# Performance work log

Hardware: AMD Instinct MI355X
Metric: run time of the kernel (lower is better)

## Reference

```python
import jax, jax.numpy as jnp
import numpy as np
import math

B, LQ, LK, D = 16, 2048, 2048, 64

def setup_inputs() -> dict:
    key = jax.random.key(0)
    kq, kk, kv, kn = jax.random.split(key, 4)
    q = jax.random.normal(kq, (B, LQ, D), dtype=jnp.float32)
    k = jax.random.normal(kk, (B, LK, D), dtype=jnp.float32)
    v = jax.random.normal(kv, (B, LK, D), dtype=jnp.float32)
    # valid lengths in [1, LK] so no row is fully masked
    valid_num = jax.random.randint(kn, (B,), 1, LK + 1, dtype=jnp.int32)
    return {"q": q, "k": k, "v": v, "valid_num": valid_num}

def reference(q, k, v, valid_num):
    d = q.shape[-1]
    # [B, LQ, LK] scores
    scores = jnp.einsum('bqd,bkd->bqk', q, k) / math.sqrt(d)
    # 1D valid_num -> same key mask for every query row (matches repeat_interleave)
    key_pos = jnp.arange(k.shape[1], dtype=valid_num.dtype)  # [LK]
    mask = key_pos[None, None, :] < valid_num[:, None, None]  # [B,1,LK] -> broadcast
    scores = jnp.where(mask, scores, -jnp.inf)
    attn = jax.nn.softmax(scores, axis=-1)
    # dropout p=0.0 -> identity (eval/deterministic reference)
    return jnp.einsum('bqk,bkd->bqd', attn, v)
```

## Files before the change

kernel.cpp:

```cpp
#include <hip/hip_runtime.h>


namespace {

constexpr int NB  = 16;
constexpr int SLQ = 2048;
constexpr int SLK = 2048;
constexpr int DH  = 64;
constexpr int KB  = 64;
constexpr int QB  = 64;

typedef _Float16 half8  __attribute__((ext_vector_type(8)));
typedef _Float16 half4  __attribute__((ext_vector_type(4)));
typedef _Float16 half2t __attribute__((ext_vector_type(2)));
typedef float    f32x4  __attribute__((ext_vector_type(4)));

__device__ inline half2t pkrtz(float a, float b) {
    return __builtin_bit_cast(half2t, __builtin_amdgcn_cvt_pkrtz(a, b));
}

__global__ __launch_bounds__(256)
void prepass(const float* __restrict__ kg, const float* __restrict__ vg,
             _Float16* __restrict__ k16, _Float16* __restrict__ v16t)
{
    __shared__ _Float16 VT[DH][72];
    const int t  = threadIdx.x;
    const int b  = blockIdx.x >> 5;
    const int kt = blockIdx.x & 31;

    {
        const size_t base = ((size_t)b * SLK + (size_t)kt * KB) * DH;
        const float* kp = kg + base + t * 16;
        f32x4 a0 = ((const f32x4*)kp)[0], a1 = ((const f32x4*)kp)[1];
        f32x4 a2 = ((const f32x4*)kp)[2], a3 = ((const f32x4*)kp)[3];
        union { half2t h2[8]; uint4 u[2]; } o;
        o.h2[0] = pkrtz(a0[0], a0[1]); o.h2[1] = pkrtz(a0[2], a0[3]);
        o.h2[2] = pkrtz(a1[0], a1[1]); o.h2[3] = pkrtz(a1[2], a1[3]);
        o.h2[4] = pkrtz(a2[0], a2[1]); o.h2[5] = pkrtz(a2[2], a2[3]);
        o.h2[6] = pkrtz(a3[0], a3[1]); o.h2[7] = pkrtz(a3[2], a3[3]);
        uint4* dst = (uint4*)(k16 + base + t * 16);
        dst[0] = o.u[0]; dst[1] = o.u[1];
    }
    {
        const int kr = t >> 2, d0 = (t & 3) * 16;
        const float* vp = vg + ((size_t)b * SLK + (size_t)kt * KB + kr) * DH + d0;
        f32x4 a0 = ((const f32x4*)vp)[0], a1 = ((const f32x4*)vp)[1];
        f32x4 a2 = ((const f32x4*)vp)[2], a3 = ((const f32x4*)vp)[3];
#pragma unroll
        for (int i = 0; i < 4; ++i) {
            VT[d0 + i][kr]      = (_Float16)a0[i];
            VT[d0 + 4 + i][kr]  = (_Float16)a1[i];
            VT[d0 + 8 + i][kr]  = (_Float16)a2[i];
            VT[d0 + 12 + i][kr] = (_Float16)a3[i];
        }
    }
    __syncthreads();
#pragma unroll
    for (int j = 0; j < 2; ++j) {
        const int chunk = t * 2 + j;
        const int d = chunk >> 3, c16 = chunk & 7;
        half8 hv = *(const half8*)&VT[d][c16 * 8];
        *(half8*)(v16t + ((size_t)b * DH + d) * SLK + (size_t)kt * KB + c16 * 8) = hv;
    }
}

__global__ __launch_bounds__(256)
void attn_fwd(const float* __restrict__ qg, const _Float16* __restrict__ k16,
              const _Float16* __restrict__ v16t, const int* __restrict__ vn,
              _Float16* __restrict__ ws_acc, float* __restrict__ ws_ml,
              int nsplit, int tps)
{
    __shared__ _Float16 Kl[KB * DH];
    __shared__ _Float16 Vt[DH * KB];

    const int t   = threadIdx.x;
    const int l   = t & 63;
    const int w   = t >> 6;
    const int q15 = l & 15;
    const int g   = l >> 4;
    const int swz = (q15 & 7) << 3;

    const int bid = blockIdx.x;
    int b, qt, s;
    if (nsplit == 4) {
        const int k3  = bid >> 8;
        const int mm  = (bid >> 4) & 15;
        const int qlo = bid & 15;
        s  = k3 & 3;
        b  = (mm + k3) & 15;
        qt = qlo | ((k3 >> 2) << 4);
    } else {
        b  = ((bid & 15) + 8 * (bid >> 8)) & 15;
        qt = (bid >> 4) & 31;
        s  = 0;
    }

    const int valid = vn[b];
    const int nkt   = (valid + KB - 1) / KB;
    const int kt0   = s * tps;
    if (kt0 >= nkt) return;
    const int kt1   = min(nkt, kt0 + tps);

    const int qrow = qt * QB + w * 16 + q15;

    const float QS = 0.18033688011112042f;

    half8 qf[2];
    {
        const float* qp = qg + ((size_t)b * SLQ + qrow) * DH;
#pragma unroll
        for (int ss = 0; ss < 2; ++ss) {
            const int d0 = 8 * g + 32 * ss;
            f32x4 x = *(const f32x4*)(qp + d0);
            f32x4 y = *(const f32x4*)(qp + d0 + 4);
            half8 h;
#pragma unroll
            for (int i = 0; i < 4; ++i) {
                h[i]     = (_Float16)(x[i] * QS);
                h[i + 4] = (_Float16)(y[i] * QS);
            }
            qf[ss] = h;
        }
    }

    f32x4 acc[4];
#pragma unroll
    for (int i = 0; i < 4; ++i) acc[i] = f32x4{0.f, 0.f, 0.f, 0.f};
    float m = -1e30f, lsum = 0.f;

    const _Float16* k16b = k16 + (size_t)b * SLK * DH;
    const _Float16* v16b = v16t + (size_t)b * DH * SLK;

    for (int kt = kt0; kt < kt1; ++kt) {
        __syncthreads();

#pragma unroll
        for (int j = 0; j < 2; ++j) {
            const int chunk = 2 * t + j;
            const int r = chunk >> 3, c16 = chunk & 7;
            const int sc = (c16 * 8) ^ ((r & 7) << 3);
            uint4 kd = *(const uint4*)(k16b + (size_t)kt * KB * DH + chunk * 8);
            *(uint4*)&Kl[r * 64 + sc] = kd;
            uint4 vd = *(const uint4*)(v16b + (size_t)r * SLK + kt * KB + c16 * 8);
            *(uint4*)&Vt[r * 64 + sc] = vd;
        }
        __syncthreads();

        f32x4 st[4];
#pragma unroll
        for (int mt = 0; mt < 4; ++mt) {
            f32x4 c = f32x4{0.f, 0.f, 0.f, 0.f};
#pragma unroll
            for (int ss = 0; ss < 2; ++ss) {
                half8 a = *(const half8*)&Kl[(16 * mt + q15) * 64 + ((8 * g + 32 * ss) ^ swz)];
                c = __builtin_amdgcn_mfma_f32_16x16x32_f16(a, qf[ss], c, 0, 0, 0);
            }
            st[mt] = c;
        }

        const int krem = valid - kt * KB;
        if (krem < KB) {
#pragma unroll
            for (int mt = 0; mt < 4; ++mt)
#pragma unroll
                for (int r = 0; r < 4; ++r)
                    if (16 * mt + 4 * g + r >= krem) st[mt][r] = -1e30f;
        }

        float tmax = -1e30f;
#pragma unroll
        for (int mt = 0; mt < 4; ++mt)
#pragma unroll
            for (int r = 0; r < 4; ++r) tmax = fmaxf(tmax, st[mt][r]);
        tmax = fmaxf(tmax, __shfl_xor(tmax, 16));
        tmax = fmaxf(tmax, __shfl_xor(tmax, 32));

        const float mn = fmaxf(m, tmax);
        const float sc = __builtin_amdgcn_exp2f(m - mn);

        float p[4][4];
        float ps = 0.f;
#pragma unroll
        for (int mt = 0; mt < 4; ++mt)
#pragma unroll
            for (int r = 0; r < 4; ++r) {
                const float e = __builtin_amdgcn_exp2f(st[mt][r] - mn);
                p[mt][r] = e;
                ps += e;
            }
        ps += __shfl_xor(ps, 16);
        ps += __shfl_xor(ps, 32);
        lsum = lsum * sc + ps;
        m = mn;
#pragma unroll
        for (int mt = 0; mt < 4; ++mt) acc[mt] *= sc;

        half2t pk[4][2];
#pragma unroll
        for (int mt = 0; mt < 4; ++mt)
#pragma unroll
            for (int rr = 0; rr < 2; ++rr)
                pk[mt][rr] = pkrtz(p[mt][2 * rr], p[mt][2 * rr + 1]);

#pragma unroll
        for (int ss = 0; ss < 2; ++ss) {
            union { half2t h2[4]; half8 v; } bf;
            bf.h2[0] = pk[2 * ss][0];
            bf.h2[1] = pk[2 * ss][1];
            bf.h2[2] = pk[2 * ss + 1][0];
            bf.h2[3] = pk[2 * ss + 1][1];
#pragma unroll
            for (int mt = 0; mt < 4; ++mt) {
                union { half4 h4[2]; half8 v; } af;
                af.h4[0] = *(const half4*)&Vt[(16 * mt + q15) * 64 + ((32 * ss + 4 * g) ^ swz)];
                af.h4[1] = *(const half4*)&Vt[(16 * mt + q15) * 64 + ((32 * ss + 16 + 4 * g) ^ swz)];
                acc[mt] = __builtin_amdgcn_mfma_f32_16x16x32_f16(af.v, bf.v, acc[mt], 0, 0, 0);
            }
        }
    }

    const float inv = 1.0f / lsum;
    const size_t row = (size_t)b * SLQ + qrow;
    _Float16* wp = ws_acc + ((size_t)s * NB * SLQ + row) * DH;
#pragma unroll
    for (int mt = 0; mt < 4; ++mt) {
        union { half2t h2[2]; uint2 u; } o;
        o.h2[0] = pkrtz(acc[mt][0] * inv, acc[mt][1] * inv);
        o.h2[1] = pkrtz(acc[mt][2] * inv, acc[mt][3] * inv);
        *(uint2*)(wp + 16 * mt + 4 * g) = o.u;
    }
    if (g == 0)
        *(float2*)(ws_ml + ((size_t)s * NB * SLQ + row) * 2) = make_float2(m, lsum);
}

__global__ __launch_bounds__(256)
void attn_combine(const _Float16* __restrict__ ws_acc, const float* __restrict__ ws_ml,
                  const int* __restrict__ vn, float* __restrict__ og,
                  int nsplit, int tps)
{
    const int tid = blockIdx.x * 256 + threadIdx.x;
    const int row = tid >> 2;
    const int dq  = (tid & 3) << 4;
    const int b   = row >> 11;

    const int valid = vn[b];
    const int nkt   = (valid + KB - 1) / KB;
    const int nact  = min(nsplit, (nkt + tps - 1) / tps);

    float M = -1e30f;
    for (int s = 0; s < nact; ++s)
        M = fmaxf(M, ws_ml[((size_t)s * NB * SLQ + row) * 2]);

    float L = 0.f;
    f32x4 o[4];
#pragma unroll
    for (int i = 0; i < 4; ++i) o[i] = f32x4{0.f, 0.f, 0.f, 0.f};

    for (int s = 0; s < nact; ++s) {
        const float2 ml = *(const float2*)(ws_ml + ((size_t)s * NB * SLQ + row) * 2);
        const float wl = __builtin_amdgcn_exp2f(ml.x - M) * ml.y;
        L += wl;
        const _Float16* ap = ws_acc + ((size_t)s * NB * SLQ + row) * DH + dq;
        half8 h0 = ((const half8*)ap)[0];
        half8 h1 = ((const half8*)ap)[1];
#pragma unroll
        for (int r = 0; r < 4; ++r) {
            o[0][r] += wl * (float)h0[r];
            o[1][r] += wl * (float)h0[4 + r];
            o[2][r] += wl * (float)h1[r];
            o[3][r] += wl * (float)h1[4 + r];
        }
    }

    const float inv = 1.0f / L;
    float* op = og + (size_t)row * DH + dq;
#pragma unroll
    for (int i = 0; i < 4; ++i) {
        f32x4 r = o[i] * inv;
        *(f32x4*)(op + 4 * i) = r;
    }
}

}

extern "C" void kernel_launch(void* const* d_in, const int* in_sizes, int n_in,
                              void* d_out, int out_size, void* d_ws, size_t ws_size,
                              hipStream_t stream)
{
    const float* q    = (const float*)d_in[0];
    const float* k    = (const float*)d_in[1];
    const float* v    = (const float*)d_in[2];
    const int*   vnum = (const int*)d_in[3];
    float* out = (float*)d_out;

    const size_t k16H = (size_t)NB * SLK * DH;
    const size_t v16H = k16H;
    const size_t rowsH = (size_t)NB * SLQ;

    int nsplit = 4;
    {
        const size_t need4 = (k16H + v16H + 4 * rowsH * DH) * 2 + 4 * rowsH * 2 * 4;
        if (ws_size < need4) nsplit = 1;
    }
    const int tps = (nsplit == 4) ? 8 : 32;

    _Float16* k16    = (_Float16*)d_ws;
    _Float16* v16t   = k16 + k16H;
    _Float16* ws_acc = v16t + v16H;
    float*    ws_ml  = (float*)(ws_acc + (size_t)nsplit * rowsH * DH);

    prepass<<<dim3(NB * (SLK / KB)), dim3(256), 0, stream>>>(k, v, k16, v16t);

    dim3 gfwd(nsplit == 4 ? 2048 : 512);
    attn_fwd<<<gfwd, dim3(256), 0, stream>>>(q, k16, v16t, vnum, ws_acc, ws_ml,
                                             nsplit, tps);

    attn_combine<<<dim3((NB * SLQ * 4) / 256), dim3(256), 0, stream>>>(
        ws_acc, ws_ml, vnum, out, nsplit, tps);
}
```

Measured before the change: 45.80 us.

## Prefetch K/V tiles into registers, lazy rescale, 8-way key split

Raises the key-dimension split from 4 to 8 (4096 blocks, 4 tiles each) and loads the next K/V tile into registers while the current tile is computed. It also skips the softmax max/rescale update when the wave-wide max increase stays within a threshold, and raises wave priority around the MFMA sections. The intent is to hide global-load latency, cut per-tile exp/multiply work and improve occupancy and load balance across batches with differing valid lengths. The cost is more workspace and combine traffic, shorter per-block loops that amortise setup less, and slightly higher register pressure.

```diff
diff --git a/kernel.cpp b/kernel.cpp
--- a/kernel.cpp
+++ b/kernel.cpp
@@ -82,13 +82,11 @@
 
     const int bid = blockIdx.x;
     int b, qt, s;
-    if (nsplit == 4) {
-        const int k3  = bid >> 8;
-        const int mm  = (bid >> 4) & 15;
-        const int qlo = bid & 15;
-        s  = k3 & 3;
-        b  = (mm + k3) & 15;
-        qt = qlo | ((k3 >> 2) << 4);
+    if (nsplit == 8) {
+        const int k4 = bid >> 8;
+        s  = k4 & 7;
+        b  = (((bid >> 4) & 15) + k4) & 15;
+        qt = (bid & 15) | ((k4 >> 3) << 4);
     } else {
         b  = ((bid & 15) + 8 * (bid >> 8)) & 15;
         qt = (bid >> 4) & 31;
@@ -131,22 +129,39 @@
     const _Float16* k16b = k16 + (size_t)b * SLK * DH;
     const _Float16* v16b = v16t + (size_t)b * DH * SLK;
 
+    const int chunk = 2 * t;
+    const int rr_   = chunk >> 3;
+    const int cc_   = chunk & 7;
+    const int scA   = (cc_ * 8) ^ ((rr_ & 7) << 3);
+    const int scB   = scA ^ 8;
+    const _Float16* ksrc = k16b + (size_t)chunk * 8;
+    const _Float16* vsrc = v16b + (size_t)rr_ * SLK + cc_ * 8;
+
+    uint4 ka, kb, va, vb;
+#define PREFETCH(KT)                                                       \
+    {                                                                      \
+        const _Float16* kp = ksrc + (size_t)(KT) * (KB * DH);              \
+        ka = ((const uint4*)kp)[0];                                        \
+        kb = ((const uint4*)kp)[1];                                        \
+        const _Float16* vp = vsrc + (size_t)(KT) * KB;                     \
+        va = ((const uint4*)vp)[0];                                        \
+        vb = ((const uint4*)vp)[1];                                        \
+    }
+
+    PREFETCH(kt0);
+
     for (int kt = kt0; kt < kt1; ++kt) {
         __syncthreads();
 
-#pragma unroll
-        for (int j = 0; j < 2; ++j) {
-            const int chunk = 2 * t + j;
-            const int r = chunk >> 3, c16 = chunk & 7;
-            const int sc = (c16 * 8) ^ ((r & 7) << 3);
-            uint4 kd = *(const uint4*)(k16b + (size_t)kt * KB * DH + chunk * 8);
-            *(uint4*)&Kl[r * 64 + sc] = kd;
-            uint4 vd = *(const uint4*)(v16b + (size_t)r * SLK + kt * KB + c16 * 8);
-            *(uint4*)&Vt[r * 64 + sc] = vd;
-        }
+        *(uint4*)&Kl[rr_ * 64 + scA] = ka;
+        *(uint4*)&Kl[rr_ * 64 + scB] = kb;
+        *(uint4*)&Vt[rr_ * 64 + scA] = va;
+        *(uint4*)&Vt[rr_ * 64 + scB] = vb;
+        if (kt + 1 < kt1) PREFETCH(kt + 1);
         __syncthreads();
 
         f32x4 st[4];
+        __builtin_amdgcn_s_setprio(1);
 #pragma unroll
         for (int mt = 0; mt < 4; ++mt) {
             f32x4 c = f32x4{0.f, 0.f, 0.f, 0.f};
@@ -157,6 +172,7 @@
             }
             st[mt] = c;
         }
+        __builtin_amdgcn_s_setprio(0);
 
         const int krem = valid - kt * KB;
         if (krem < KB) {
@@ -167,33 +183,38 @@
                     if (16 * mt + 4 * g + r >= krem) st[mt][r] = -1e30f;
         }
 
-        float tmax = -1e30f;
-#pragma unroll
-        for (int mt = 0; mt < 4; ++mt)
-#pragma unroll
-            for (int r = 0; r < 4; ++r) tmax = fmaxf(tmax, st[mt][r]);
+        float x0 = fmaxf(fmaxf(st[0][0], st[0][1]), fmaxf(st[0][2], st[0][3]));
+        float x1 = fmaxf(fmaxf(st[1][0], st[1][1]), fmaxf(st[1][2], st[1][3]));
+        float x2 = fmaxf(fmaxf(st[2][0], st[2][1]), fmaxf(st[2][2], st[2][3]));
+        float x3 = fmaxf(fmaxf(st[3][0], st[3][1]), fmaxf(st[3][2], st[3][3]));
+        float tmax = fmaxf(fmaxf(x0, x1), fmaxf(x2, x3));
         tmax = fmaxf(tmax, __shfl_xor(tmax, 16));
         tmax = fmaxf(tmax, __shfl_xor(tmax, 32));
 
-        const float mn = fmaxf(m, tmax);
-        const float sc = __builtin_amdgcn_exp2f(m - mn);
+        if (!__all(tmax - m <= 12.0f)) {
+            const float mn = fmaxf(m, tmax);
+            const float sc = __builtin_amdgcn_exp2f(m - mn);
+            lsum *= sc;
+#pragma unroll
+            for (int mt = 0; mt < 4; ++mt) acc[mt] *= sc;
+            m = mn;
+        }
 
         float p[4][4];
-        float ps = 0.f;
 #pragma unroll
         for (int mt = 0; mt < 4; ++mt)
 #pragma unroll
-            for (int r = 0; r < 4; ++r) {
-                const float e = __builtin_amdgcn_exp2f(st[mt][r] - mn);
-                p[mt][r] = e;
-                ps += e;
-            }
+            for (int r = 0; r < 4; ++r)
+                p[mt][r] = __builtin_amdgcn_exp2f(st[mt][r] - m);
+
+        float s0 = (p[0][0] + p[0][1]) + (p[0][2] + p[0][3]);
+        float s1 = (p[1][0] + p[1][1]) + (p[1][2] + p[1][3]);
+        float s2 = (p[2][0] + p[2][1]) + (p[2][2] + p[2][3]);
+        float s3 = (p[3][0] + p[3][1]) + (p[3][2] + p[3][3]);
+        float ps = (s0 + s1) + (s2 + s3);
         ps += __shfl_xor(ps, 16);
         ps += __shfl_xor(ps, 32);
-        lsum = lsum * sc + ps;
-        m = mn;
-#pragma unroll
-        for (int mt = 0; mt < 4; ++mt) acc[mt] *= sc;
+        lsum += ps;
 
         half2t pk[4][2];
 #pragma unroll
@@ -202,6 +223,7 @@
             for (int rr = 0; rr < 2; ++rr)
                 pk[mt][rr] = pkrtz(p[mt][2 * rr], p[mt][2 * rr + 1]);
 
+        __builtin_amdgcn_s_setprio(1);
 #pragma unroll
         for (int ss = 0; ss < 2; ++ss) {
             union { half2t h2[4]; half8 v; } bf;
@@ -217,7 +239,9 @@
                 acc[mt] = __builtin_amdgcn_mfma_f32_16x16x32_f16(af.v, bf.v, acc[mt], 0, 0, 0);
             }
         }
-    }
+        __builtin_amdgcn_s_setprio(0);
+    }
+#undef PREFETCH
 
     const float inv = 1.0f / lsum;
     const size_t row = (size_t)b * SLQ + qrow;
@@ -293,16 +317,17 @@
     const int*   vnum = (const int*)d_in[3];
     float* out = (float*)d_out;
 
-    const size_t k16H = (size_t)NB * SLK * DH;
-    const size_t v16H = k16H;
+    const size_t k16H  = (size_t)NB * SLK * DH;
+    const size_t v16H  = k16H;
     const size_t rowsH = (size_t)NB * SLQ;
 
-    int nsplit = 4;
+    int nsplit = 8;
     {
-        const size_t need4 = (k16H + v16H + 4 * rowsH * DH) * 2 + 4 * rowsH * 2 * 4;
-        if (ws_size < need4) nsplit = 1;
-    }
-    const int tps = (nsplit == 4) ? 8 : 32;
+        const size_t need8 = (k16H + v16H + (size_t)8 * rowsH * DH) * 2
+                           + (size_t)8 * rowsH * 2 * 4;
+        if (ws_size < need8) nsplit = 1;
+    }
+    const int tps = (nsplit == 8) ? 4 : 32;
 
     _Float16* k16    = (_Float16*)d_ws;
     _Float16* v16t   = k16 + k16H;
@@ -311,7 +336,7 @@
 
     prepass<<<dim3(NB * (SLK / KB)), dim3(256), 0, stream>>>(k, v, k16, v16t);
 
-    dim3 gfwd(nsplit == 4 ? 2048 : 512);
+    dim3 gfwd(nsplit == 8 ? 4096 : 512);
     attn_fwd<<<gfwd, dim3(256), 0, stream>>>(q, k16, v16t, vnum, ws_acc, ws_ml,
                                              nsplit, tps);
 
```

After: 43.87 us. 1.04x faster.
